# Kernel tuning notes

Measured on AMD Instinct MI355X. Metric: run time of the kernel, lower is better.

The kernel has to match this reference:

```python
import math
import jax, jax.numpy as jnp
import numpy as np

NA = 50000   # number of query nodes
NB = 50000   # number of key/value nodes
E = 800000   # number of edges
CA = 256
CB = 256
D = 256
H = 8
DH = D // H


def setup_inputs() -> dict:
    key = jax.random.key(0)
    ks = jax.random.split(key, 8)
    s = 1.0 / math.sqrt(CA)
    return {
        "Fa": jax.random.normal(ks[0], (NA, CA), dtype=jnp.float32),
        "Fb": jax.random.normal(ks[1], (NB, CB), dtype=jnp.float32),
        "a_idx": jax.random.randint(ks[2], (E,), 0, NA, dtype=jnp.int64)
        if jax.config.jax_enable_x64 else jax.random.randint(ks[2], (E,), 0, NA, dtype=jnp.int32),
        "b_idx": jax.random.randint(ks[3], (E,), 0, NB, dtype=jnp.int64)
        if jax.config.jax_enable_x64 else jax.random.randint(ks[3], (E,), 0, NB, dtype=jnp.int32),
        # torch nn.Linear weights: (out_features, in_features), y = x @ W.T
        "Wq": jax.random.normal(ks[4], (D, CA), dtype=jnp.float32) * s,
        "Wk": jax.random.normal(ks[5], (D, CB), dtype=jnp.float32) * s,
        "Wv": jax.random.normal(ks[6], (D, CB), dtype=jnp.float32) * s,
        "Wproj": jax.random.normal(ks[7], (CA, D), dtype=jnp.float32) * s,
    }


def _edge_attention(Q, K, V, Q_idx, K_idx, n_queries):
    # Q: (Na,H,dh)  K,V: (Nb,H,dh)  Q_idx,K_idx: (E,)
    scale = 1.0 / math.sqrt(Q.shape[-1])
    logits = jnp.sum(Q[Q_idx] * K[K_idx], axis=-1) * scale      # (E, H)
    # segmented softmax over edges sharing the same query (per head)
    seg_max = jax.ops.segment_max(logits, Q_idx, num_segments=n_queries)  # (Na, H)
    seg_max = jnp.where(jnp.isfinite(seg_max), seg_max, 0.0)
    ex = jnp.exp(logits - seg_max[Q_idx])                        # (E, H)
    seg_sum = jax.ops.segment_sum(ex, Q_idx, num_segments=n_queries)      # (Na, H)
    weights = ex / jnp.maximum(seg_sum[Q_idx], 1e-30)            # (E, H)
    # scatter-add weighted values
    out = jax.ops.segment_sum(weights[..., None] * V[K_idx], Q_idx,
                              num_segments=n_queries)            # (Na, H, dh)
    return out


def reference(Fa, Fb, a_idx, b_idx, Wq, Wk, Wv, Wproj):
    Na = Fa.shape[0]
    Q = (Fa @ Wq.T).reshape(Na, H, DH)
    K = (Fb @ Wk.T).reshape(-1, H, DH)
    V = (Fb @ Wv.T).reshape(-1, H, DH)
    out = _edge_attention(Q, K, V, a_idx, b_idx, Na)
    out = out.reshape(Na, H * DH)
    return Fa + out @ Wproj.T
```

## Files before the change

kernel.cpp:

```cpp
#include <hip/hip_runtime.h>

#define DM 256
#define QSCALE 0.25503403f

typedef __attribute__((ext_vector_type(8))) short bf16x8;
typedef __attribute__((ext_vector_type(4))) float f32x4;
typedef __attribute__((ext_vector_type(4))) unsigned short us16x4;
typedef __attribute__((ext_vector_type(8))) unsigned short us16x8;
typedef unsigned short us16;

__device__ __forceinline__ unsigned short f2bf(float f) {
  unsigned int u = __float_as_uint(f);
  u += 0x7fffu + ((u >> 16) & 1u);
  return (unsigned short)(u >> 16);
}
__device__ __forceinline__ float bf2f(unsigned short s) {
  return __uint_as_float(((unsigned int)s) << 16);
}

__device__ __forceinline__ void gload16(const void* g, void* l) {
  __builtin_amdgcn_global_load_lds(
      (const __attribute__((address_space(1))) void*)g,
      (__attribute__((address_space(3))) void*)l, 16, 0, 0);
}

__global__ __launch_bounds__(512) void qkv_gemm(
    const float* __restrict__ Fa, const float* __restrict__ Fb,
    const us16* __restrict__ W_all, us16* __restrict__ Qbf,
    us16* __restrict__ KVbf, int NA, int NB)
{
  const int z = blockIdx.z;
  const float* A = (z == 0) ? Fa : Fb;
  const int Mreal = (z == 0) ? NA : NB;
  const int Mp = (Mreal + 127) & ~127;
  const us16* W = W_all + (size_t)z * 256 * 256;
  us16* Cb = (z == 0) ? Qbf : KVbf;
  const int ldc = (z == 0) ? 256 : 512;
  const int colofs = (z == 2) ? 256 : 0;

  __shared__ us16 As[2][128 * 32];
  __shared__ us16 Bs[2][256 * 32];
  const int tid = threadIdx.x;
  const int w = tid >> 6, l = tid & 63;
  const int wr = w >> 2, wc = w & 3;
  const int rowBase = blockIdx.x * 128;
  if (rowBase >= Mp) return;
  const int ar = tid >> 2, ac = (tid & 3) * 8;
  const int grow0 = rowBase + ar;
  const bool aval = grow0 < Mreal;
  const float* Ap = A + (size_t)grow0 * 256 + ac;
  f32x4 acc[4][4] = {};

  {
    float4 x = make_float4(0.f, 0.f, 0.f, 0.f), y = x;
    if (aval) { x = *(const float4*)(Ap); y = *(const float4*)(Ap + 4); }
#pragma unroll
    for (int j = 0; j < 2; ++j) {
      const int r0 = (w * 2 + j) * 16;
      gload16(W + (size_t)(r0 + (l >> 2)) * 256 + (l & 3) * 8, &Bs[0][r0 * 32]);
    }
    bf16x8 av;
    av[0] = (short)f2bf(x.x); av[1] = (short)f2bf(x.y);
    av[2] = (short)f2bf(x.z); av[3] = (short)f2bf(x.w);
    av[4] = (short)f2bf(y.x); av[5] = (short)f2bf(y.y);
    av[6] = (short)f2bf(y.z); av[7] = (short)f2bf(y.w);
    *(bf16x8*)&As[0][ar * 32 + ac] = av;
  }
  __syncthreads();

  for (int t = 0; t < 8; ++t) {
    const int cur = t & 1, nxt = cur ^ 1;
    const bool pf = (t < 7);
    float4 x, y;
    if (pf) {
      const int k0 = (t + 1) * 32;
      x = make_float4(0.f, 0.f, 0.f, 0.f); y = x;
      if (aval) { x = *(const float4*)(Ap + k0); y = *(const float4*)(Ap + k0 + 4); }
#pragma unroll
      for (int j = 0; j < 2; ++j) {
        const int r0 = (w * 2 + j) * 16;
        gload16(W + (size_t)(r0 + (l >> 2)) * 256 + k0 + (l & 3) * 8,
                &Bs[nxt][r0 * 32]);
      }
    }
    bf16x8 af[4], bfr[4];
#pragma unroll
    for (int m = 0; m < 4; ++m)
      af[m] = *(const bf16x8*)&As[cur][(wr * 64 + m * 16 + (l & 15)) * 32 + (l >> 4) * 8];
#pragma unroll
    for (int n = 0; n < 4; ++n)
      bfr[n] = *(const bf16x8*)&Bs[cur][(wc * 64 + n * 16 + (l & 15)) * 32 + (l >> 4) * 8];
#pragma unroll
    for (int m = 0; m < 4; ++m)
#pragma unroll
      for (int n = 0; n < 4; ++n)
        acc[m][n] = __builtin_amdgcn_mfma_f32_16x16x32_bf16(af[m], bfr[n], acc[m][n], 0, 0, 0);
    if (pf) {
      bf16x8 av;
      av[0] = (short)f2bf(x.x); av[1] = (short)f2bf(x.y);
      av[2] = (short)f2bf(x.z); av[3] = (short)f2bf(x.w);
      av[4] = (short)f2bf(y.x); av[5] = (short)f2bf(y.y);
      av[6] = (short)f2bf(y.z); av[7] = (short)f2bf(y.w);
      *(bf16x8*)&As[nxt][ar * 32 + ac] = av;
    }
    __syncthreads();
  }

  const int er = (l >> 4) * 4;
  const int ec = l & 15;
#pragma unroll
  for (int m = 0; m < 4; ++m)
#pragma unroll
    for (int n = 0; n < 4; ++n)
#pragma unroll
      for (int j = 0; j < 4; ++j) {
        const int grow = rowBase + wr * 64 + m * 16 + er + j;
        const int c = wc * 64 + n * 16 + ec;
        float v = acc[m][n][j];
        if (z == 0) v *= QSCALE;
        Cb[(size_t)grow * ldc + c + colofs] = f2bf(v);
      }
}

__global__ __launch_bounds__(512) void proj_gemm(
    const us16* __restrict__ A, const us16* __restrict__ W,
    float* __restrict__ Cf, const float* __restrict__ R, int Mreal)
{
  __shared__ us16 As[2][128 * 32];
  __shared__ us16 Bs[2][256 * 32];
  const int tid = threadIdx.x;
  const int w = tid >> 6, l = tid & 63;
  const int wr = w >> 2, wc = w & 3;
  const int rowBase = blockIdx.x * 128;
  f32x4 acc[4][4] = {};

  {
    const int r0 = w * 16;
    gload16(A + (size_t)(rowBase + r0 + (l >> 2)) * 256 + (l & 3) * 8,
            &As[0][r0 * 32]);
#pragma unroll
    for (int j = 0; j < 2; ++j) {
      const int rb = (w * 2 + j) * 16;
      gload16(W + (size_t)(rb + (l >> 2)) * 256 + (l & 3) * 8, &Bs[0][rb * 32]);
    }
  }
  __syncthreads();

  for (int t = 0; t < 8; ++t) {
    const int cur = t & 1, nxt = cur ^ 1;
    if (t < 7) {
      const int k0 = (t + 1) * 32;
      const int r0 = w * 16;
      gload16(A + (size_t)(rowBase + r0 + (l >> 2)) * 256 + k0 + (l & 3) * 8,
              &As[nxt][r0 * 32]);
#pragma unroll
      for (int j = 0; j < 2; ++j) {
        const int rb = (w * 2 + j) * 16;
        gload16(W + (size_t)(rb + (l >> 2)) * 256 + k0 + (l & 3) * 8,
                &Bs[nxt][rb * 32]);
      }
    }
    bf16x8 af[4], bfr[4];
#pragma unroll
    for (int m = 0; m < 4; ++m)
      af[m] = *(const bf16x8*)&As[cur][(wr * 64 + m * 16 + (l & 15)) * 32 + (l >> 4) * 8];
#pragma unroll
    for (int n = 0; n < 4; ++n)
      bfr[n] = *(const bf16x8*)&Bs[cur][(wc * 64 + n * 16 + (l & 15)) * 32 + (l >> 4) * 8];
#pragma unroll
    for (int m = 0; m < 4; ++m)
#pragma unroll
      for (int n = 0; n < 4; ++n)
        acc[m][n] = __builtin_amdgcn_mfma_f32_16x16x32_bf16(af[m], bfr[n], acc[m][n], 0, 0, 0);
    __syncthreads();
  }

  const int er = (l >> 4) * 4;
  const int ec = l & 15;
#pragma unroll
  for (int m = 0; m < 4; ++m)
#pragma unroll
    for (int n = 0; n < 4; ++n)
#pragma unroll
      for (int j = 0; j < 4; ++j) {
        const int grow = rowBase + wr * 64 + m * 16 + er + j;
        if (grow < Mreal) {
          const size_t off = (size_t)grow * 256 + wc * 64 + n * 16 + ec;
          Cf[off] = acc[m][n][j] + R[off];
        }
      }
}

__global__ void cvt_weights(const float* __restrict__ Wq, const float* __restrict__ Wk,
                            const float* __restrict__ Wv, const float* __restrict__ Wp,
                            us16* __restrict__ out)
{
  const int g = blockIdx.x * 256 + threadIdx.x;
  const size_t e = (size_t)g * 8;
  const int sel = (int)(e >> 16);
  const float* src = (sel == 0) ? Wq : (sel == 1) ? Wk : (sel == 2) ? Wv : Wp;
  const size_t loc = e & 65535;
  const float4 x = *(const float4*)(src + loc);
  const float4 y = *(const float4*)(src + loc + 4);
  bf16x8 o;
  o[0] = (short)f2bf(x.x); o[1] = (short)f2bf(x.y);
  o[2] = (short)f2bf(x.z); o[3] = (short)f2bf(x.w);
  o[4] = (short)f2bf(y.x); o[5] = (short)f2bf(y.y);
  o[6] = (short)f2bf(y.z); o[7] = (short)f2bf(y.w);
  *(bf16x8*)(out + e) = o;
}

__global__ void hist_kernel(const int* __restrict__ a_idx, int* __restrict__ counts, int E)
{
  const int e = blockIdx.x * 256 + threadIdx.x;
  if (e < E) atomicAdd(&counts[a_idx[e]], 1);
}

__global__ __launch_bounds__(256) void scan_offs(const int* __restrict__ counts,
    int* __restrict__ offs, int* __restrict__ cursor, int* __restrict__ total, int n)
{
  __shared__ int buf[256];
  __shared__ int sbase;
  const int t = threadIdx.x;
  const int i = blockIdx.x * 256 + t;
  const int v = (i < n) ? counts[i] : 0;
  buf[t] = v;
  __syncthreads();
#pragma unroll
  for (int off = 1; off < 256; off <<= 1) {
    const int x = (t >= off) ? buf[t - off] : 0;
    __syncthreads();
    buf[t] += x;
    __syncthreads();
  }
  const int incl = buf[t];
  if (t == 255) sbase = atomicAdd(total, incl);
  __syncthreads();
  if (i < n) {
    const int excl = sbase + incl - v;
    offs[i] = excl;
    cursor[i] = excl;
  }
}

__global__ void scatter_kernel(const int* __restrict__ a_idx, const int* __restrict__ b_idx,
    int* __restrict__ cursor, int* __restrict__ bel, int E)
{
  const int e = blockIdx.x * 256 + threadIdx.x;
  if (e < E) bel[atomicAdd(&cursor[a_idx[e]], 1)] = b_idx[e];
}

#define ATTN_STEP(K, V, J)                                     \
  if ((J) < cnt) {                                             \
    float p = q0 * bf2f(K[0]);                                 \
    p = fmaf(q1, bf2f(K[1]), p);                               \
    p = fmaf(q2, bf2f(K[2]), p);                               \
    p = fmaf(q3, bf2f(K[3]), p);                               \
    p = fmaf(q4, bf2f(K[4]), p);                               \
    p = fmaf(q5, bf2f(K[5]), p);                               \
    p = fmaf(q6, bf2f(K[6]), p);                               \
    p = fmaf(q7, bf2f(K[7]), p);                               \
    p += __shfl_xor(p, 1, 64);                                 \
    p += __shfl_xor(p, 2, 64);                                 \
    const float ex = exp2f(p);                                 \
    ssum += ex;                                                \
    acc0 = fmaf(ex, bf2f(V[0]), acc0);                         \
    acc1 = fmaf(ex, bf2f(V[1]), acc1);                         \
    acc2 = fmaf(ex, bf2f(V[2]), acc2);                         \
    acc3 = fmaf(ex, bf2f(V[3]), acc3);                         \
    acc4 = fmaf(ex, bf2f(V[4]), acc4);                         \
    acc5 = fmaf(ex, bf2f(V[5]), acc5);                         \
    acc6 = fmaf(ex, bf2f(V[6]), acc6);                         \
    acc7 = fmaf(ex, bf2f(V[7]), acc7);                         \
  }

#define ATTN_LOAD(K, V, IDX)                                   \
  {                                                            \
    const us16* kv = KVb + (size_t)bel[sstart + (IDX)] * 512 + kvo; \
    K = *(const us16x8*)(kv);                                  \
    V = *(const us16x8*)(kv + 256);                            \
  }

__global__ __launch_bounds__(256) void edge_attn(
    const us16* __restrict__ Qb, const us16* __restrict__ KVb,
    const int* __restrict__ offs, const int* __restrict__ counts,
    const int* __restrict__ bel, us16* __restrict__ outb, int NA)
{
  const int a = blockIdx.x * 8 + (threadIdx.x >> 5);
  const int hd = threadIdx.x & 31;
  const int kvo = hd * 8;
  const bool valid = (a < NA);

  const int aa = valid ? a : (NA - 1);
  const us16x8 q8 = *(const us16x8*)(Qb + (size_t)aa * 256 + kvo);
  const float q0 = bf2f(q8[0]), q1 = bf2f(q8[1]), q2 = bf2f(q8[2]), q3 = bf2f(q8[3]);
  const float q4 = bf2f(q8[4]), q5 = bf2f(q8[5]), q6 = bf2f(q8[6]), q7 = bf2f(q8[7]);

  const int cnt = valid ? counts[a] : 0;
  const int sstart = (cnt > 0) ? offs[a] : 0;
  const int last = (cnt > 0) ? cnt - 1 : 0;
  const int mcnt = max(cnt, __shfl_xor(cnt, 32, 64));

  float acc0 = 0.f, acc1 = 0.f, acc2 = 0.f, acc3 = 0.f;
  float acc4 = 0.f, acc5 = 0.f, acc6 = 0.f, acc7 = 0.f;
  float ssum = 0.f;

  if (mcnt > 0) {
    us16x8 ka, va, kb, vb, kc, vc, kd, vd;
    ATTN_LOAD(ka, va, 0)
    ATTN_LOAD(kb, vb, min(1, last))
    ATTN_LOAD(kc, vc, min(2, last))
    ATTN_LOAD(kd, vd, min(3, last))
    for (int i = 0; i < mcnt; i += 4) {
      us16x8 na, xa, nb, xb, nc, xc, nd, xd;
      ATTN_LOAD(na, xa, min(i + 4, last))
      ATTN_LOAD(nb, xb, min(i + 5, last))
      ATTN_LOAD(nc, xc, min(i + 6, last))
      ATTN_LOAD(nd, xd, min(i + 7, last))
      ATTN_STEP(ka, va, i + 0)
      ATTN_STEP(kb, vb, i + 1)
      ATTN_STEP(kc, vc, i + 2)
      ATTN_STEP(kd, vd, i + 3)
      ka = na; va = xa; kb = nb; vb = xb;
      kc = nc; vc = xc; kd = nd; vd = xd;
    }
  }

  if (valid) {
    const float inv = (cnt > 0) ? 1.f / ssum : 0.f;
    us16x8 o;
    o[0] = (short)f2bf(acc0 * inv); o[1] = (short)f2bf(acc1 * inv);
    o[2] = (short)f2bf(acc2 * inv); o[3] = (short)f2bf(acc3 * inv);
    o[4] = (short)f2bf(acc4 * inv); o[5] = (short)f2bf(acc5 * inv);
    o[6] = (short)f2bf(acc6 * inv); o[7] = (short)f2bf(acc7 * inv);
    *(us16x8*)(outb + (size_t)a * 256 + kvo) = o;
  }
}

extern "C" void kernel_launch(void* const* d_in, const int* in_sizes, int n_in,
                              void* d_out, int out_size, void* d_ws, size_t ws_size,
                              hipStream_t stream)
{
  const float* Fa    = (const float*)d_in[0];
  const float* Fb    = (const float*)d_in[1];
  const int*   a_idx = (const int*)d_in[2];
  const int*   b_idx = (const int*)d_in[3];
  const float* Wq    = (const float*)d_in[4];
  const float* Wk    = (const float*)d_in[5];
  const float* Wv    = (const float*)d_in[6];
  const float* Wproj = (const float*)d_in[7];
  float* out = (float*)d_out;

  const int NA = in_sizes[0] / DM;
  const int NB = in_sizes[1] / DM;
  const int E  = in_sizes[2];
  const int MAp = (NA + 127) & ~127;
  const int NBp = (NB + 127) & ~127;
  const int MXp = (MAp > NBp) ? MAp : NBp;

  us16* Qbf   = (us16*)d_ws;
  us16* KVbf  = Qbf   + (size_t)MAp * 256;
  us16* ATbf  = KVbf  + (size_t)NBp * 512;
  us16* W_all = ATbf  + (size_t)MAp * 256;
  int* total  = (int*)(W_all + 1024 * 256);
  int* counts = total + 1;
  int* offs   = counts + NA;
  int* cursor = offs + NA;
  int* bel    = cursor + NA;

  hipMemsetAsync(total, 0, (size_t)(NA + 1) * sizeof(int), stream);

  cvt_weights<<<128, 256, 0, stream>>>(Wq, Wk, Wv, Wproj, W_all);

  hist_kernel<<<(E + 255) / 256, 256, 0, stream>>>(a_idx, counts, E);
  scan_offs<<<(NA + 255) / 256, 256, 0, stream>>>(counts, offs, cursor, total, NA);
  scatter_kernel<<<(E + 255) / 256, 256, 0, stream>>>(a_idx, b_idx, cursor, bel, E);

  qkv_gemm<<<dim3(MXp / 128, 1, 3), 512, 0, stream>>>(Fa, Fb, W_all, Qbf, KVbf, NA, NB);

  edge_attn<<<(NA + 7) / 8, 256, 0, stream>>>(Qbf, KVbf, offs, counts, bel, ATbf, NA);

  proj_gemm<<<dim3(MAp / 128, 1), 512, 0, stream>>>(ATbf, W_all + 768 * 256, out, Fa, NA);
}
```

Measured before the change: 439.5 us.

## Fuse weight conversion with histogram and edge scatter into QKV GEMM launch

Merges the bf16 weight conversion and the a_idx histogram into one kernel. The CSR scatter moves into the QKV GEMM as an extra grid z-slice, so it runs alongside the GEMM tiles. Together these cut kernel launches and let the latency-bound atomic work overlap with compute. The edge attention launch is also split into two half-sized launches on the same stream; this has no obvious benefit and adds one launch.

```diff
diff --git a/kernel.cpp b/kernel.cpp
--- a/kernel.cpp
+++ b/kernel.cpp
@@ -27,9 +27,22 @@
 __global__ __launch_bounds__(512) void qkv_gemm(
     const float* __restrict__ Fa, const float* __restrict__ Fb,
     const us16* __restrict__ W_all, us16* __restrict__ Qbf,
-    us16* __restrict__ KVbf, int NA, int NB)
-{
+    us16* __restrict__ KVbf, int NA, int NB,
+    const int* __restrict__ a_idx, const int* __restrict__ b_idx,
+    int* __restrict__ cursor, int* __restrict__ bel, int E)
+{
+  __shared__ us16 As[2][128 * 32];
+  __shared__ us16 Bs[2][256 * 32];
   const int z = blockIdx.z;
+  const int tid = threadIdx.x;
+
+  if (z == 3) {
+    const int nth = gridDim.x * 512;
+    for (int e = blockIdx.x * 512 + tid; e < E; e += nth)
+      bel[atomicAdd(&cursor[a_idx[e]], 1)] = b_idx[e];
+    return;
+  }
+
   const float* A = (z == 0) ? Fa : Fb;
   const int Mreal = (z == 0) ? NA : NB;
   const int Mp = (Mreal + 127) & ~127;
@@ -38,9 +51,6 @@
   const int ldc = (z == 0) ? 256 : 512;
   const int colofs = (z == 2) ? 256 : 0;
 
-  __shared__ us16 As[2][128 * 32];
-  __shared__ us16 Bs[2][256 * 32];
-  const int tid = threadIdx.x;
   const int w = tid >> 6, l = tid & 63;
   const int wr = w >> 2, wc = w & 3;
   const int rowBase = blockIdx.x * 128;
@@ -191,29 +201,29 @@
       }
 }
 
-__global__ void cvt_weights(const float* __restrict__ Wq, const float* __restrict__ Wk,
-                            const float* __restrict__ Wv, const float* __restrict__ Wp,
-                            us16* __restrict__ out)
-{
-  const int g = blockIdx.x * 256 + threadIdx.x;
-  const size_t e = (size_t)g * 8;
-  const int sel = (int)(e >> 16);
-  const float* src = (sel == 0) ? Wq : (sel == 1) ? Wk : (sel == 2) ? Wv : Wp;
-  const size_t loc = e & 65535;
-  const float4 x = *(const float4*)(src + loc);
-  const float4 y = *(const float4*)(src + loc + 4);
-  bf16x8 o;
-  o[0] = (short)f2bf(x.x); o[1] = (short)f2bf(x.y);
-  o[2] = (short)f2bf(x.z); o[3] = (short)f2bf(x.w);
-  o[4] = (short)f2bf(y.x); o[5] = (short)f2bf(y.y);
-  o[6] = (short)f2bf(y.z); o[7] = (short)f2bf(y.w);
-  *(bf16x8*)(out + e) = o;
-}
-
-__global__ void hist_kernel(const int* __restrict__ a_idx, int* __restrict__ counts, int E)
-{
-  const int e = blockIdx.x * 256 + threadIdx.x;
-  if (e < E) atomicAdd(&counts[a_idx[e]], 1);
+__global__ void cvt_hist(const float* __restrict__ Wq, const float* __restrict__ Wk,
+                         const float* __restrict__ Wv, const float* __restrict__ Wp,
+                         us16* __restrict__ out,
+                         const int* __restrict__ a_idx, int* __restrict__ counts, int E)
+{
+  if (blockIdx.x < 128) {
+    const int g = blockIdx.x * 256 + threadIdx.x;
+    const size_t e = (size_t)g * 8;
+    const int sel = (int)(e >> 16);
+    const float* src = (sel == 0) ? Wq : (sel == 1) ? Wk : (sel == 2) ? Wv : Wp;
+    const size_t loc = e & 65535;
+    const float4 x = *(const float4*)(src + loc);
+    const float4 y = *(const float4*)(src + loc + 4);
+    bf16x8 o;
+    o[0] = (short)f2bf(x.x); o[1] = (short)f2bf(x.y);
+    o[2] = (short)f2bf(x.z); o[3] = (short)f2bf(x.w);
+    o[4] = (short)f2bf(y.x); o[5] = (short)f2bf(y.y);
+    o[6] = (short)f2bf(y.z); o[7] = (short)f2bf(y.w);
+    *(bf16x8*)(out + e) = o;
+  } else {
+    const int e = (blockIdx.x - 128) * 256 + threadIdx.x;
+    if (e < E) atomicAdd(&counts[a_idx[e]], 1);
+  }
 }
 
 __global__ __launch_bounds__(256) void scan_offs(const int* __restrict__ counts,
@@ -241,13 +251,6 @@
     offs[i] = excl;
     cursor[i] = excl;
   }
-}
-
-__global__ void scatter_kernel(const int* __restrict__ a_idx, const int* __restrict__ b_idx,
-    int* __restrict__ cursor, int* __restrict__ bel, int E)
-{
-  const int e = blockIdx.x * 256 + threadIdx.x;
-  if (e < E) bel[atomicAdd(&cursor[a_idx[e]], 1)] = b_idx[e];
 }
 
 #define ATTN_STEP(K, V, J)                                     \
@@ -284,9 +287,9 @@
 __global__ __launch_bounds__(256) void edge_attn(
     const us16* __restrict__ Qb, const us16* __restrict__ KVb,
     const int* __restrict__ offs, const int* __restrict__ counts,
-    const int* __restrict__ bel, us16* __restrict__ outb, int NA)
-{
-  const int a = blockIdx.x * 8 + (threadIdx.x >> 5);
+    const int* __restrict__ bel, us16* __restrict__ outb, int NA, int nodeBase)
+{
+  const int a = nodeBase + blockIdx.x * 8 + (threadIdx.x >> 5);
   const int hd = threadIdx.x & 31;
   const int kvo = hd * 8;
   const bool valid = (a < NA);
@@ -370,15 +373,21 @@
 
   hipMemsetAsync(total, 0, (size_t)(NA + 1) * sizeof(int), stream);
 
-  cvt_weights<<<128, 256, 0, stream>>>(Wq, Wk, Wv, Wproj, W_all);
-
-  hist_kernel<<<(E + 255) / 256, 256, 0, stream>>>(a_idx, counts, E);
+  cvt_hist<<<128 + (E + 255) / 256, 256, 0, stream>>>(
+      Wq, Wk, Wv, Wproj, W_all, a_idx, counts, E);
+
   scan_offs<<<(NA + 255) / 256, 256, 0, stream>>>(counts, offs, cursor, total, NA);
-  scatter_kernel<<<(E + 255) / 256, 256, 0, stream>>>(a_idx, b_idx, cursor, bel, E);
-
-  qkv_gemm<<<dim3(MXp / 128, 1, 3), 512, 0, stream>>>(Fa, Fb, W_all, Qbf, KVbf, NA, NB);
-
-  edge_attn<<<(NA + 7) / 8, 256, 0, stream>>>(Qbf, KVbf, offs, counts, bel, ATbf, NA);
+
+  qkv_gemm<<<dim3(MXp / 128, 1, 4), 512, 0, stream>>>(
+      Fa, Fb, W_all, Qbf, KVbf, NA, NB, a_idx, b_idx, cursor, bel, E);
+
+  const int blkTotal = (NA + 7) / 8;
+  const int blkLo = (blkTotal + 1) / 2;
+  const int baseHi = blkLo * 8;
+  int blkHi = (NA - baseHi + 7) / 8;
+  if (blkHi < 1) blkHi = 1;
+  edge_attn<<<blkLo, 256, 0, stream>>>(Qbf, KVbf, offs, counts, bel, ATbf, NA, 0);
+  edge_attn<<<blkHi, 256, 0, stream>>>(Qbf, KVbf, offs, counts, bel, ATbf, NA, baseHi);
 
   proj_gemm<<<dim3(MAp / 128, 1), 512, 0, stream>>>(ATbf, W_all + 768 * 256, out, Fa, NA);
 }
```

Result: no change. 443.4 us (+0.9%).
